# Kernel optimization log

Measured on AMD Instinct MI355X. Metric: run time of the kernel, lower is better.

The kernel has to match this reference:

```python
import math
import jax, jax.numpy as jnp
import numpy as np

D_MODEL = 1024
N_HEADS = 16
HEAD_DIM = D_MODEL // N_HEADS
D_FF = 4096
LN_EPS = 1e-5


def _layer_norm(x, g, b):
    mu = jnp.mean(x, axis=-1, keepdims=True)
    var = jnp.var(x, axis=-1, keepdims=True)
    return (x - mu) * jax.lax.rsqrt(var + LN_EPS) * g + b


def setup_inputs() -> dict:
    key = jax.random.key(0)
    ks = jax.random.split(key, 8)
    s = 0.02
    d, dff = D_MODEL, D_FF
    return {
        "src": jax.random.normal(ks[0], (2, 2048, d), dtype=jnp.float32),
        "in_proj_w": jax.random.normal(ks[1], (3 * d, d), dtype=jnp.float32) * s,
        "in_proj_b": jnp.zeros((3 * d,), dtype=jnp.float32),
        "out_w": jax.random.normal(ks[2], (d, d), dtype=jnp.float32) * s,
        "out_b": jnp.zeros((d,), dtype=jnp.float32),
        "lin1_w": jax.random.normal(ks[3], (dff, d), dtype=jnp.float32) * s,
        "lin1_b": jnp.zeros((dff,), dtype=jnp.float32),
        "lin2_w": jax.random.normal(ks[4], (d, dff), dtype=jnp.float32) * s,
        "lin2_b": jnp.zeros((d,), dtype=jnp.float32),
        "ln1_g": jnp.ones((d,), dtype=jnp.float32),
        "ln1_b": jnp.zeros((d,), dtype=jnp.float32),
        "ln2_g": jnp.ones((d,), dtype=jnp.float32),
        "ln2_b": jnp.zeros((d,), dtype=jnp.float32),
    }


def reference(src, in_proj_w, in_proj_b, out_w, out_b, lin1_w, lin1_b,
              lin2_w, lin2_b, ln1_g, ln1_b, ln2_g, ln2_b):
    B, S, d = src.shape
    # QKV projections (in_proj_weight split at d, then kv split)
    q = src @ in_proj_w[:d].T + in_proj_b[:d]              # [B,S,d]
    kv = src @ in_proj_w[d:].T + in_proj_b[d:]             # [B,S,2d]
    q = q.reshape(B, S, N_HEADS, HEAD_DIM)
    kv = kv.reshape(B, S, 2, N_HEADS, HEAD_DIM)
    k, v = kv[:, :, 0], kv[:, :, 1]
    softmax_scale = 1.0 / math.sqrt(HEAD_DIM)
    scores = jnp.einsum('bthd,bshd->bhts', q, k) * softmax_scale  # [B,H,Sq,Skv]
    # 'distribute': softmax over the QUERY dimension (dim=-2)
    attention = jax.nn.softmax(scores, axis=-2)
    post = jnp.einsum('bhts,bshd->bthd', attention, v)     # [B,Sq,H,hd]
    # post-attention activation 'gelu' (torch exact gelu)
    post = jax.nn.gelu(post, approximate=False)
    # attention_scale == 'sqrt': divide by sqrt(kv_len)
    post = post / math.sqrt(S)
    attn_out = post.reshape(B, S, d) @ out_w.T + out_b
    # post-norm residual structure (pre_norm=False, dropout=0)
    x = _layer_norm(src + attn_out, ln1_g, ln1_b)
    ff = jax.nn.gelu(x @ lin1_w.T + lin1_b, approximate=False) @ lin2_w.T + lin2_b
    return _layer_norm(x + ff, ln2_g, ln2_b)
```

## Files before the change

### kernel.cpp

```cpp
#include <hip/hip_runtime.h>
#include <hip/hip_bf16.h>
#include <math.h>


using bf16x8 = __attribute__((ext_vector_type(8))) short;
using f32x4  = __attribute__((ext_vector_type(4))) float;

__device__ inline f32x4 mfma16(bf16x8 a, bf16x8 b, f32x4 c) {
    return __builtin_amdgcn_mfma_f32_16x16x32_bf16(a, b, c, 0, 0, 0);
}

__device__ inline ushort f2bf(float f) {
    union { float f; unsigned u; } x; x.f = f;
    unsigned r = x.u + 0x7fffu + ((x.u >> 16) & 1u);
    return (ushort)(r >> 16);
}

__device__ inline float bf2f(ushort u) {
    union { unsigned u; float f; } x; x.u = ((unsigned)u) << 16; return x.f;
}

__device__ inline float gelu_fast(float v) {
    float u = v * (1.5957691216f + 0.0713548162f * v * v);
    float e = __expf(u);
    return v * (e / (e + 1.0f));
}

__device__ __forceinline__ void gl2lds16(const ushort* g, ushort* l) {
    __builtin_amdgcn_global_load_lds(
        (const __attribute__((address_space(1))) unsigned int*)g,
        (__attribute__((address_space(3))) unsigned int*)l,
        16, 0, 0);
}

__global__ __launch_bounds__(256) void cvt_all(const float4* __restrict__ s0,
                                               const float4* __restrict__ s1,
                                               const float4* __restrict__ s2,
                                               const float4* __restrict__ s3,
                                               const float4* __restrict__ s4,
                                               ushort4* __restrict__ out) {
    int i = blockIdx.x * 256 + threadIdx.x;
    const float4* p;
    int off;
    if (i < 1048576)      { p = s0; off = i; }
    else if (i < 1835008) { p = s1; off = i - 1048576; }
    else if (i < 2097152) { p = s2; off = i - 1835008; }
    else if (i < 3145728) { p = s3; off = i - 2097152; }
    else                  { p = s4; off = i - 3145728; }
    float4 v = p[off];
    ushort4 o;
    o.x = f2bf(v.x); o.y = f2bf(v.y); o.z = f2bf(v.z); o.w = f2bf(v.w);
    out[i] = o;
}

__global__ __launch_bounds__(256) void gemm_bt(
    const ushort* __restrict__ A, const ushort* __restrict__ Bw,
    const float* __restrict__ bias, int M, int N, int K, int kLen, int mode,
    ushort* __restrict__ ob0, ushort* __restrict__ ob1, ushort* __restrict__ ob2) {
    __shared__ ushort As[128 * 32];
    __shared__ ushort Bs[128 * 32];
    int tid = threadIdx.x, lane = tid & 63, w = tid >> 6;
    int wm = w >> 1, wn = w & 1;
    int bm = blockIdx.y * 128, bn = blockIdx.x * 128;
    int kz = blockIdx.z;
    int q4 = lane >> 4, l15 = lane & 15;
    f32x4 acc[4][4] = {};

    int srow = w * 16 + (lane >> 2);
    int scg = lane & 3;
    const ushort* Ab = A + (size_t)bm * K + (size_t)kz * kLen;
    const ushort* Bb = Bw + (size_t)bn * K + (size_t)kz * kLen;
    const ushort* gA0 = Ab + (size_t)srow * K + scg * 8;
    const ushort* gA1 = Ab + (size_t)(64 + srow) * K + scg * 8;
    const ushort* gB0 = Bb + (size_t)srow * K + scg * 8;
    const ushort* gB1 = Bb + (size_t)(64 + srow) * K + scg * 8;
    ushort* lA0 = As + w * 512;
    ushort* lA1 = As + 2048 + w * 512;
    ushort* lB0 = Bs + w * 512;
    ushort* lB1 = Bs + 2048 + w * 512;

    const ushort* aP[4];
    const ushort* bP[4];
#pragma unroll
    for (int mi = 0; mi < 4; mi++)
        aP[mi] = As + (wm * 64 + mi * 16 + l15) * 32 + q4 * 8;
#pragma unroll
    for (int ni = 0; ni < 4; ni++)
        bP[ni] = Bs + (wn * 64 + ni * 16 + l15) * 32 + q4 * 8;

    for (int k0 = 0; k0 < kLen; k0 += 32) {
        __syncthreads();
        gl2lds16(gA0 + k0, lA0);
        gl2lds16(gA1 + k0, lA1);
        gl2lds16(gB0 + k0, lB0);
        gl2lds16(gB1 + k0, lB1);
        __syncthreads();
        bf16x8 af[4], bfr[4];
#pragma unroll
        for (int mi = 0; mi < 4; mi++) af[mi] = *(const bf16x8*)aP[mi];
#pragma unroll
        for (int ni = 0; ni < 4; ni++) bfr[ni] = *(const bf16x8*)bP[ni];
#pragma unroll
        for (int mi = 0; mi < 4; mi++)
#pragma unroll
            for (int ni = 0; ni < 4; ni++)
                acc[mi][ni] = mfma16(af[mi], bfr[ni], acc[mi][ni]);
    }

    int r0 = bm + wm * 64, c0 = bn + wn * 64;
#pragma unroll
    for (int mi = 0; mi < 4; mi++) {
#pragma unroll
        for (int ni = 0; ni < 4; ni++) {
            int colg = c0 + ni * 16 + l15;
            float bv = (mode == 3) ? 0.f : bias[colg];
#pragma unroll
            for (int r = 0; r < 4; r++) {
                int rowg = r0 + mi * 16 + q4 * 4 + r;
                float v = acc[mi][ni][r] + bv;
                if (mode == 0) {
                    if (colg < 1024) {
                        ob0[(size_t)rowg * 1024 + colg] = f2bf(v);
                    } else if (colg < 2048) {
                        ob1[(size_t)rowg * 1024 + (colg - 1024)] = f2bf(v);
                    } else {
                        ob2[(size_t)rowg * 1024 + (colg - 2048)] = f2bf(v);
                    }
                } else if (mode == 2) {
                    ob0[(size_t)rowg * N + colg] = f2bf(gelu_fast(v));
                } else {
                    ob0[(size_t)kz * M * N + (size_t)rowg * N + colg] = f2bf(v);
                }
            }
        }
    }
}

__global__ __launch_bounds__(256) void attn_colsum(const ushort* __restrict__ qb,
                                                   const ushort* __restrict__ kb,
                                                   float* __restrict__ ninv) {
    __shared__ ushort Qs[64 * 72];
    int tid = threadIdx.x, lane = tid & 63, w = tid >> 6;
    int bh = blockIdx.x >> 4, sblk = blockIdx.x & 15;
    int b = bh >> 4, h = bh & 15;
    int q4 = lane >> 4, l15 = lane & 15;
    const ushort* qbase = qb + (size_t)(b * 2048) * 1024 + h * 64;
    const ushort* kbase = kb + (size_t)(b * 2048) * 1024 + h * 64;
    int s_base = sblk * 128 + w * 32;

    bf16x8 ka[2][2];
#pragma unroll
    for (int mi = 0; mi < 2; mi++) {
        const ushort* kp = kbase + (size_t)(s_base + mi * 16 + l15) * 1024 + q4 * 8;
        ka[mi][0] = *(const bf16x8*)(kp);
        ka[mi][1] = *(const bf16x8*)(kp + 32);
    }
    float acc[2][4] = {};

    int sr = tid >> 3;
    int sc = (tid & 7) * 8;
    for (int t0 = 0; t0 < 2048; t0 += 64) {
        uint4 g0 = *(const uint4*)(qbase + (size_t)(t0 + sr) * 1024 + sc);
        uint4 g1 = *(const uint4*)(qbase + (size_t)(t0 + 32 + sr) * 1024 + sc);
        __syncthreads();
        *(uint4*)&Qs[sr * 72 + sc] = g0;
        *(uint4*)&Qs[(32 + sr) * 72 + sc] = g1;
        __syncthreads();
#pragma unroll
        for (int tsub = 0; tsub < 4; tsub++) {
            bf16x8 bq0 = *(const bf16x8*)&Qs[(tsub * 16 + l15) * 72 + q4 * 8];
            bf16x8 bq1 = *(const bf16x8*)&Qs[(tsub * 16 + l15) * 72 + 32 + q4 * 8];
#pragma unroll
            for (int mi = 0; mi < 2; mi++) {
                f32x4 d = {0.f, 0.f, 0.f, 0.f};
                d = mfma16(ka[mi][0], bq0, d);
                d = mfma16(ka[mi][1], bq1, d);
#pragma unroll
                for (int r = 0; r < 4; r++)
                    acc[mi][r] += __expf(d[r] * 0.125f);
            }
        }
    }
#pragma unroll
    for (int mi = 0; mi < 2; mi++)
#pragma unroll
        for (int r = 0; r < 4; r++) {
            float v = acc[mi][r];
            v += __shfl_xor(v, 1); v += __shfl_xor(v, 2);
            v += __shfl_xor(v, 4); v += __shfl_xor(v, 8);
            if (l15 == 0)
                ninv[(size_t)bh * 2048 + s_base + mi * 16 + q4 * 4 + r] = 1.f / v;
        }
}

__global__ __launch_bounds__(256) void vt_scale_transpose(const ushort* __restrict__ vrow,
                                                          const float* __restrict__ ninv,
                                                          ushort* __restrict__ vt) {
    __shared__ ushort T[64 * 72];
    int tid = threadIdx.x;
    int bh = blockIdx.x >> 5, sch = blockIdx.x & 31;
    int b = bh >> 4, h = bh & 15;
    int s0 = sch * 64;
    int sl = tid >> 3, dh = (tid & 7) * 8;
#pragma unroll
    for (int rep = 0; rep < 2; rep++) {
        int s = sl + rep * 32;
        float n = ninv[(size_t)bh * 2048 + s0 + s];
        const ushort* p = vrow + (size_t)(b * 2048 + s0 + s) * 1024 + h * 64 + dh;
        ushort4 u0 = ((const ushort4*)p)[0];
        ushort4 u1 = ((const ushort4*)p)[1];
        ushort4 o0, o1;
        o0.x = f2bf(bf2f(u0.x) * n); o0.y = f2bf(bf2f(u0.y) * n);
        o0.z = f2bf(bf2f(u0.z) * n); o0.w = f2bf(bf2f(u0.w) * n);
        o1.x = f2bf(bf2f(u1.x) * n); o1.y = f2bf(bf2f(u1.y) * n);
        o1.z = f2bf(bf2f(u1.z) * n); o1.w = f2bf(bf2f(u1.w) * n);
        *(ushort4*)&T[s * 72 + dh] = o0;
        *(ushort4*)&T[s * 72 + dh + 4] = o1;
    }
    __syncthreads();
    int dhl = tid >> 3, soff = (tid & 7) * 8;
#pragma unroll
    for (int rep = 0; rep < 2; rep++) {
        int d = dhl + rep * 32;
        ushort tmp[8];
#pragma unroll
        for (int j = 0; j < 8; j++) tmp[j] = T[(soff + j) * 72 + d];
        *(uint4*)(vt + ((size_t)bh * 64 + d) * 2048 + s0 + soff) = *(uint4*)tmp;
    }
}

__global__ __launch_bounds__(256) void attn_pv(const ushort* __restrict__ qb,
                                               const ushort* __restrict__ kb,
                                               const ushort* __restrict__ vt,
                                               ushort* __restrict__ post) {
    __shared__ ushort Ks[64 * 72];
    __shared__ ushort Vs[64 * 72];
    __shared__ ushort Ps[4][32 * 72];
    int tid = threadIdx.x, lane = tid & 63, w = tid >> 6;
    int bh = blockIdx.x >> 4, tblk = blockIdx.x & 15;
    int b = bh >> 4, h = bh & 15;
    int q4 = lane >> 4, l15 = lane & 15;
    const ushort* qbase = qb + (size_t)(b * 2048) * 1024 + h * 64;
    const ushort* kbase = kb + (size_t)(b * 2048) * 1024 + h * 64;
    const ushort* vtb = vt + (size_t)bh * 64 * 2048;
    int t_base = tblk * 128 + w * 32;

    bf16x8 aq[2][2];
#pragma unroll
    for (int mi = 0; mi < 2; mi++) {
        const ushort* qp = qbase + (size_t)(t_base + mi * 16 + l15) * 1024 + q4 * 8;
        aq[mi][0] = *(const bf16x8*)(qp);
        aq[mi][1] = *(const bf16x8*)(qp + 32);
    }
    f32x4 oacc[2][4] = {};
    ushort* myP = Ps[w];

    int sr = tid >> 3;
    int sc = (tid & 7) * 8;
    for (int s0 = 0; s0 < 2048; s0 += 64) {
        uint4 k0g = *(const uint4*)(kbase + (size_t)(s0 + sr) * 1024 + sc);
        uint4 k1g = *(const uint4*)(kbase + (size_t)(s0 + 32 + sr) * 1024 + sc);
        uint4 v0g = *(const uint4*)(vtb + (size_t)sr * 2048 + s0 + sc);
        uint4 v1g = *(const uint4*)(vtb + (size_t)(32 + sr) * 2048 + s0 + sc);
        __syncthreads();
        *(uint4*)&Ks[sr * 72 + sc] = k0g;
        *(uint4*)&Ks[(32 + sr) * 72 + sc] = k1g;
        *(uint4*)&Vs[sr * 72 + sc] = v0g;
        *(uint4*)&Vs[(32 + sr) * 72 + sc] = v1g;
        __syncthreads();
#pragma unroll
        for (int ssub = 0; ssub < 4; ssub++) {
            bf16x8 bk0 = *(const bf16x8*)&Ks[(ssub * 16 + l15) * 72 + q4 * 8];
            bf16x8 bk1 = *(const bf16x8*)&Ks[(ssub * 16 + l15) * 72 + 32 + q4 * 8];
#pragma unroll
            for (int mi = 0; mi < 2; mi++) {
                f32x4 d = {0.f, 0.f, 0.f, 0.f};
                d = mfma16(aq[mi][0], bk0, d);
                d = mfma16(aq[mi][1], bk1, d);
#pragma unroll
                for (int r = 0; r < 4; r++)
                    myP[(mi * 16 + q4 * 4 + r) * 72 + ssub * 16 + l15] =
                        f2bf(__expf(d[r] * 0.125f));
            }
        }
        bf16x8 bv[4][2];
#pragma unroll
        for (int ni = 0; ni < 4; ni++) {
            bv[ni][0] = *(const bf16x8*)&Vs[(ni * 16 + l15) * 72 + q4 * 8];
            bv[ni][1] = *(const bf16x8*)&Vs[(ni * 16 + l15) * 72 + 32 + q4 * 8];
        }
#pragma unroll
        for (int mi = 0; mi < 2; mi++) {
            bf16x8 ap0 = *(const bf16x8*)&myP[(mi * 16 + l15) * 72 + q4 * 8];
            bf16x8 ap1 = *(const bf16x8*)&myP[(mi * 16 + l15) * 72 + 32 + q4 * 8];
#pragma unroll
            for (int ni = 0; ni < 4; ni++) {
                oacc[mi][ni] = mfma16(ap0, bv[ni][0], oacc[mi][ni]);
                oacc[mi][ni] = mfma16(ap1, bv[ni][1], oacc[mi][ni]);
            }
        }
    }
#pragma unroll
    for (int mi = 0; mi < 2; mi++)
#pragma unroll
        for (int ni = 0; ni < 4; ni++)
#pragma unroll
            for (int r = 0; r < 4; r++) {
                int t = t_base + mi * 16 + q4 * 4 + r;
                float g = gelu_fast(oacc[mi][ni][r]) * 0.022097086912079608f;
                post[(size_t)(b * 2048 + t) * 1024 + h * 64 + ni * 16 + l15] = f2bf(g);
            }
}

__global__ __launch_bounds__(256) void ln_comb4(const ushort* __restrict__ parts,
                                                const float* __restrict__ bias,
                                                const float* __restrict__ res,
                                                const float* __restrict__ gw,
                                                const float* __restrict__ bw,
                                                ushort* __restrict__ outb,
                                                float* __restrict__ outf) {
    const size_t PLANE = (size_t)4096 * 1024;
    int row = blockIdx.x, tid = threadIdx.x;
    int lane = tid & 63, wid = tid >> 6;
    size_t off = (size_t)row * 1024 + tid * 4;
    float4 r = *(const float4*)(res + off);
    float4 bb = *(const float4*)(bias + tid * 4);
    float4 v;
    v.x = r.x + bb.x; v.y = r.y + bb.y; v.z = r.z + bb.z; v.w = r.w + bb.w;
#pragma unroll
    for (int p = 0; p < 4; p++) {
        ushort4 u = *(const ushort4*)(parts + p * PLANE + off);
        v.x += bf2f(u.x); v.y += bf2f(u.y); v.z += bf2f(u.z); v.w += bf2f(u.w);
    }
    float s = v.x + v.y + v.z + v.w;
    float ss = v.x * v.x + v.y * v.y + v.z * v.z + v.w * v.w;
    for (int m = 1; m < 64; m <<= 1) { s += __shfl_xor(s, m); ss += __shfl_xor(ss, m); }
    __shared__ float red[8];
    if (lane == 0) { red[wid] = s; red[wid + 4] = ss; }
    __syncthreads();
    s = red[0] + red[1] + red[2] + red[3];
    ss = red[4] + red[5] + red[6] + red[7];
    float mu = s * (1.f / 1024.f);
    float var = ss * (1.f / 1024.f) - mu * mu;
    float inv = rsqrtf(var + 1e-5f);
    float4 gv = *(const float4*)(gw + tid * 4);
    float4 bv = *(const float4*)(bw + tid * 4);
    float o0 = (v.x - mu) * inv * gv.x + bv.x;
    float o1 = (v.y - mu) * inv * gv.y + bv.y;
    float o2 = (v.z - mu) * inv * gv.z + bv.z;
    float o3 = (v.w - mu) * inv * gv.w + bv.w;
    if (outf) {
        float4 o; o.x = o0; o.y = o1; o.z = o2; o.w = o3;
        *(float4*)(outf + off) = o;
    }
    if (outb) {
        ushort4 o; o.x = f2bf(o0); o.y = f2bf(o1); o.z = f2bf(o2); o.w = f2bf(o3);
        *(ushort4*)(outb + off) = o;
    }
}

extern "C" void kernel_launch(void* const* d_in, const int* in_sizes, int n_in,
                              void* d_out, int out_size, void* d_ws, size_t ws_size,
                              hipStream_t stream) {
    const float* src  = (const float*)d_in[0];
    const float* w_in = (const float*)d_in[1];
    const float* b_in = (const float*)d_in[2];
    const float* w_o  = (const float*)d_in[3];
    const float* b_o  = (const float*)d_in[4];
    const float* w1   = (const float*)d_in[5];
    const float* b1   = (const float*)d_in[6];
    const float* w2   = (const float*)d_in[7];
    const float* b2   = (const float*)d_in[8];
    const float* g1   = (const float*)d_in[9];
    const float* be1  = (const float*)d_in[10];
    const float* g2   = (const float*)d_in[11];
    const float* be2  = (const float*)d_in[12];
    float* out = (float*)d_out;

    const size_t M = 4096;
    char* wsp = (char*)d_ws;
    size_t off = 0;
    auto alloc = [&](size_t bytes) -> void* {
        void* p = wsp + off;
        off = (off + bytes + 255) & ~(size_t)255;
        return p;
    };
    ushort* src_bf  = (ushort*)alloc(M * 1024 * 2);
    ushort* win_bf  = (ushort*)alloc(3072 * 1024 * 2);
    ushort* wout_bf = (ushort*)alloc(1024 * 1024 * 2);
    ushort* w1_bf   = (ushort*)alloc(4096 * 1024 * 2);
    ushort* w2_bf   = (ushort*)alloc((size_t)1024 * 4096 * 2);
    ushort* q_bf    = (ushort*)alloc(M * 1024 * 2);
    ushort* k_bf    = (ushort*)alloc(M * 1024 * 2);
    ushort* vt_bf   = (ushort*)alloc(M * 1024 * 2);
    float*  ninv    = (float*)alloc(2 * 16 * 2048 * 4);
    ushort* post_bf = (ushort*)alloc(M * 1024 * 2);
    ushort* part    = (ushort*)alloc(4 * M * 1024 * 2);
    ushort* x_bf    = (ushort*)alloc(M * 1024 * 2);
    float*  x_f32   = (float*)alloc(M * 1024 * 4);
    ushort* h1_bf   = (ushort*)alloc(M * 4096 * 2);
    ushort* v_row   = part;

    cvt_all<<<16384, 256, 0, stream>>>((const float4*)src, (const float4*)w_in,
                                       (const float4*)w_o, (const float4*)w1,
                                       (const float4*)w2, (ushort4*)src_bf);

    gemm_bt<<<dim3(24, 32, 1), 256, 0, stream>>>(src_bf, win_bf, b_in, 4096, 3072, 1024, 1024, 0,
                                                 q_bf, k_bf, v_row);

    attn_colsum<<<512, 256, 0, stream>>>(q_bf, k_bf, ninv);
    vt_scale_transpose<<<1024, 256, 0, stream>>>(v_row, ninv, vt_bf);
    attn_pv<<<512, 256, 0, stream>>>(q_bf, k_bf, vt_bf, post_bf);

    gemm_bt<<<dim3(8, 32, 4), 256, 0, stream>>>(post_bf, wout_bf, b_o, 4096, 1024, 1024, 256, 3,
                                                part, nullptr, nullptr);
    ln_comb4<<<4096, 256, 0, stream>>>(part, b_o, src, g1, be1, x_bf, x_f32);

    gemm_bt<<<dim3(32, 32, 1), 256, 0, stream>>>(x_bf, w1_bf, b1, 4096, 4096, 1024, 1024, 2,
                                                 h1_bf, nullptr, nullptr);
    gemm_bt<<<dim3(8, 32, 4), 256, 0, stream>>>(h1_bf, w2_bf, b2, 4096, 1024, 4096, 1024, 3,
                                                part, nullptr, nullptr);
    ln_comb4<<<4096, 256, 0, stream>>>(part, b2, x_f32, g2, be2, nullptr, out);
}
```

Measured before the change: 484.8 us.

## Deepen GEMM K-step to 64 with two LDS stages and swizzle block order

The GEMM main loop now loads two 32-wide K slices per barrier pair into two LDS buffers, which halves the number of __syncthreads per K and gives more MFMA work per sync. Block indices are also remapped in groups of 8 along M when the grid height is divisible by 8, to improve L2 locality of shared A/B tiles. This doubles LDS use per block, which may lower occupancy, and it assumes kLen is a multiple of 64.

```diff
diff --git a/kernel.cpp b/kernel.cpp
--- a/kernel.cpp
+++ b/kernel.cpp
@@ -57,11 +57,20 @@
     const ushort* __restrict__ A, const ushort* __restrict__ Bw,
     const float* __restrict__ bias, int M, int N, int K, int kLen, int mode,
     ushort* __restrict__ ob0, ushort* __restrict__ ob1, ushort* __restrict__ ob2) {
-    __shared__ ushort As[128 * 32];
-    __shared__ ushort Bs[128 * 32];
+    __shared__ ushort As[2][128 * 32];
+    __shared__ ushort Bs[2][128 * 32];
     int tid = threadIdx.x, lane = tid & 63, w = tid >> 6;
     int wm = w >> 1, wn = w & 1;
-    int bm = blockIdx.y * 128, bn = blockIdx.x * 128;
+
+    int Nx = gridDim.x, Ny = gridDim.y;
+    int bx = blockIdx.x, by = blockIdx.y;
+    if ((Ny & 7) == 0) {
+        int i = bx + Nx * by;
+        int c = i & 7, j = i >> 3;
+        bx = j % Nx;
+        by = c * (Ny >> 3) + j / Nx;
+    }
+    int bm = by * 128, bn = bx * 128;
     int kz = blockIdx.z;
     int q4 = lane >> 4, l15 = lane & 15;
     f32x4 acc[4][4] = {};
@@ -74,37 +83,46 @@
     const ushort* gA1 = Ab + (size_t)(64 + srow) * K + scg * 8;
     const ushort* gB0 = Bb + (size_t)srow * K + scg * 8;
     const ushort* gB1 = Bb + (size_t)(64 + srow) * K + scg * 8;
-    ushort* lA0 = As + w * 512;
-    ushort* lA1 = As + 2048 + w * 512;
-    ushort* lB0 = Bs + w * 512;
-    ushort* lB1 = Bs + 2048 + w * 512;
-
-    const ushort* aP[4];
-    const ushort* bP[4];
-#pragma unroll
-    for (int mi = 0; mi < 4; mi++)
-        aP[mi] = As + (wm * 64 + mi * 16 + l15) * 32 + q4 * 8;
-#pragma unroll
-    for (int ni = 0; ni < 4; ni++)
-        bP[ni] = Bs + (wn * 64 + ni * 16 + l15) * 32 + q4 * 8;
-
-    for (int k0 = 0; k0 < kLen; k0 += 32) {
-        __syncthreads();
-        gl2lds16(gA0 + k0, lA0);
-        gl2lds16(gA1 + k0, lA1);
-        gl2lds16(gB0 + k0, lB0);
-        gl2lds16(gB1 + k0, lB1);
-        __syncthreads();
-        bf16x8 af[4], bfr[4];
-#pragma unroll
-        for (int mi = 0; mi < 4; mi++) af[mi] = *(const bf16x8*)aP[mi];
-#pragma unroll
-        for (int ni = 0; ni < 4; ni++) bfr[ni] = *(const bf16x8*)bP[ni];
-#pragma unroll
-        for (int mi = 0; mi < 4; mi++)
+    ushort* lA00 = As[0] + w * 512;
+    ushort* lA10 = As[0] + 2048 + w * 512;
+    ushort* lB00 = Bs[0] + w * 512;
+    ushort* lB10 = Bs[0] + 2048 + w * 512;
+    ushort* lA01 = As[1] + w * 512;
+    ushort* lA11 = As[1] + 2048 + w * 512;
+    ushort* lB01 = Bs[1] + w * 512;
+    ushort* lB11 = Bs[1] + 2048 + w * 512;
+
+    const ushort* aB[2] = { &As[0][(wm * 64 + l15) * 32 + q4 * 8],
+                            &As[1][(wm * 64 + l15) * 32 + q4 * 8] };
+    const ushort* bB[2] = { &Bs[0][(wn * 64 + l15) * 32 + q4 * 8],
+                            &Bs[1][(wn * 64 + l15) * 32 + q4 * 8] };
+
+    for (int k0 = 0; k0 < kLen; k0 += 64) {
+        __syncthreads();
+        gl2lds16(gA0 + k0, lA00);
+        gl2lds16(gA1 + k0, lA10);
+        gl2lds16(gB0 + k0, lB00);
+        gl2lds16(gB1 + k0, lB10);
+        gl2lds16(gA0 + k0 + 32, lA01);
+        gl2lds16(gA1 + k0 + 32, lA11);
+        gl2lds16(gB0 + k0 + 32, lB01);
+        gl2lds16(gB1 + k0 + 32, lB11);
+        __syncthreads();
+#pragma unroll
+        for (int u = 0; u < 2; u++) {
+            bf16x8 af[4], bfr[4];
+#pragma unroll
+            for (int mi = 0; mi < 4; mi++)
+                af[mi] = *(const bf16x8*)(aB[u] + mi * 512);
 #pragma unroll
             for (int ni = 0; ni < 4; ni++)
-                acc[mi][ni] = mfma16(af[mi], bfr[ni], acc[mi][ni]);
+                bfr[ni] = *(const bf16x8*)(bB[u] + ni * 512);
+#pragma unroll
+            for (int mi = 0; mi < 4; mi++)
+#pragma unroll
+                for (int ni = 0; ni < 4; ni++)
+                    acc[mi][ni] = mfma16(af[mi], bfr[ni], acc[mi][ni]);
+        }
     }
 
     int r0 = bm + wm * 64, c0 = bn + wn * 64;
```

New measurement: 458.7 us. 5.4% less time.
